# Optimization experiments

Hardware: AMD Instinct MI355X
Metric: run time of the kernel (lower is better)

Reference implementation:

```python
import jax, jax.numpy as jnp
import numpy as np

D_MODEL = 512
N_HEADS = 8
D_K = D_MODEL // N_HEADS
WINDOW = 64
SCALE = 1.0 / np.sqrt(D_K)


def setup_inputs() -> dict:
    key = jax.random.key(0)
    ks = jax.random.split(key, 9)
    B, S = 1, 2048
    s = 1.0 / np.sqrt(D_MODEL)
    inp = {
        "x": jax.random.normal(ks[0], (B, S, D_MODEL), dtype=jnp.float32),
        "Wq": jax.random.normal(ks[1], (D_MODEL, D_MODEL), dtype=jnp.float32) * s,
        "bq": jnp.zeros((D_MODEL,), dtype=jnp.float32),
        "Wk": jax.random.normal(ks[2], (D_MODEL, D_MODEL), dtype=jnp.float32) * s,
        "bk": jnp.zeros((D_MODEL,), dtype=jnp.float32),
        "Wv": jax.random.normal(ks[3], (D_MODEL, D_MODEL), dtype=jnp.float32) * s,
        "bv": jnp.zeros((D_MODEL,), dtype=jnp.float32),
        "Wo": jax.random.normal(ks[4], (D_MODEL, D_MODEL), dtype=jnp.float32) * s,
        "bo": jnp.zeros((D_MODEL,), dtype=jnp.float32),
    }
    return inp


def reference(x, Wq, bq, Wk, bk, Wv, bv, Wo, bo):
    B, S, _ = x.shape
    # projections (torch Linear: x @ W.T + b); split heads -> [B,S,H,dk]
    q = (x @ Wq.T + bq).reshape(B, S, N_HEADS, D_K)
    k = (x @ Wk.T + bk).reshape(B, S, N_HEADS, D_K)
    v = (x @ Wv.T + bv).reshape(B, S, N_HEADS, D_K)

    # banded window indices: position i attends to [i-W, i+W]
    L = 2 * WINDOW + 1
    offsets = jnp.arange(L) - WINDOW                    # [L]
    pos = jnp.arange(S)[:, None] + offsets[None, :]     # [S, L]
    valid = (pos >= 0) & (pos < S)                      # [S, L]
    posc = jnp.clip(pos, 0, S - 1)

    k_w = k[:, posc]                                    # [B, S, L, H, dk]
    v_w = v[:, posc]                                    # [B, S, L, H, dk]

    scores = jnp.einsum("bshd,bslhd->bhsl", q, k_w) * SCALE
    scores = jnp.where(valid[None, None, :, :], scores, -jnp.inf)
    attn = jax.nn.softmax(scores, axis=-1)              # [B, H, S, L]
    out = jnp.einsum("bhsl,bslhd->bshd", attn, v_w)     # [B, S, H, dk]
    out = out.reshape(B, S, D_MODEL)
    return out @ Wo.T + bo
```

## Files before the change

### kernel.cpp

```cpp
#include <hip/hip_runtime.h>
#include <hip/hip_bf16.h>
#include <math.h>

#define S_LEN  2048
#define DMODEL 512
#define NHEADS 8
#define DK     64
#define WIN    64

static constexpr float SCALE = 0.125f;

typedef short bf16x8 __attribute__((ext_vector_type(8)));
typedef float f32x4  __attribute__((ext_vector_type(4)));

__device__ __forceinline__ short bfh(float v)
{
    __hip_bfloat16 b = __float2bfloat16(v);
    return *reinterpret_cast<short*>(&b);
}
__device__ __forceinline__ float bf2f(short s)
{
    __hip_bfloat16 b = *reinterpret_cast<__hip_bfloat16*>(&s);
    return __bfloat162float(b);
}
__device__ __forceinline__ void split1(float v, short& h, short& l)
{
    h = bfh(v);
    l = bfh(v - bf2f(h));
}

__device__ __forceinline__ void dma16(const void* g, void* l)
{
    __builtin_amdgcn_global_load_lds(
        (const __attribute__((address_space(1))) unsigned int*)g,
        (__attribute__((address_space(3))) unsigned int*)l, 16, 0, 0);
}

__global__ __launch_bounds__(256)
void prep(const float* __restrict__ x,
          const float* __restrict__ wq, const float* __restrict__ wk,
          const float* __restrict__ wv, const float* __restrict__ wo,
          short* __restrict__ xh, short* __restrict__ xl,
          short* __restrict__ wqb, short* __restrict__ wkb,
          short* __restrict__ wvb, short* __restrict__ wob)
{
    const int z = blockIdx.z;
    if (z == 0) {
        for (int i = blockIdx.x * 256 + threadIdx.x; i < 262144; i += gridDim.x * 256) {
            const float4 v = ((const float4*)x)[i];
            short4 h4, l4;
            split1(v.x, h4.x, l4.x);
            split1(v.y, h4.y, l4.y);
            split1(v.z, h4.z, l4.z);
            split1(v.w, h4.w, l4.w);
            ((short4*)xh)[i] = h4;
            ((short4*)xl)[i] = l4;
        }
    } else {
        const float* s; short* d;
        switch (z) {
            case 1:  s = wq; d = wqb; break;
            case 2:  s = wk; d = wkb; break;
            case 3:  s = wv; d = wvb; break;
            default: s = wo; d = wob; break;
        }
        for (int i = blockIdx.x * 256 + threadIdx.x; i < 65536; i += gridDim.x * 256) {
            const float4 v = ((const float4*)s)[i];
            short4 o;
            o.x = bfh(v.x); o.y = bfh(v.y); o.z = bfh(v.z); o.w = bfh(v.w);
            ((short4*)d)[i] = o;
        }
    }
}

__global__ __launch_bounds__(128)
void gemm_qkv7(const short* __restrict__ xh, const short* __restrict__ xl,
               const short* __restrict__ wqb, const short* __restrict__ wkb,
               const short* __restrict__ wvb,
               const float* __restrict__ bq, const float* __restrict__ bk,
               const float* __restrict__ bv,
               short* __restrict__ qb, short* __restrict__ kb,
               short* __restrict__ vbt)
{
    __shared__ __align__(16) short sW[64 * 128];

    const int z = blockIdx.z;
    const short* Bg   = (z == 0) ? wqb : (z == 1) ? wkb : wvb;
    const float* bias = (z == 0) ? bq  : (z == 1) ? bk  : bv;
    const int row0 = blockIdx.y * 32;
    const int col0 = blockIdx.x * 64;
    const int tid  = threadIdx.x;
    const int lane = tid & 63;
    const int wv   = tid >> 6;
    const int col  = lane & 15;
    const int quad = lane >> 4;
    const int m    = row0 + wv * 16 + col;

    f32x4 acc[4];
#pragma unroll
    for (int nj = 0; nj < 4; ++nj)
        acc[nj] = (f32x4)0.0f;

    for (int ph = 0; ph < 4; ++ph) {
        __syncthreads();
        for (int i = wv; i < 16; i += 2) {
            const int r = i * 4 + (lane >> 4);
            const int c = lane & 15;
            const int j = c ^ (r & 7);
            dma16(Bg + (size_t)(col0 + r) * 512 + ph * 128 + j * 8, sW + i * 512);
        }
        __syncthreads();

#pragma unroll
        for (int kc = 0; kc < 4; ++kc) {
            const size_t aoff = (size_t)m * 512 + ph * 128 + kc * 32 + quad * 8;
            const bf16x8 ah = *(const bf16x8*)(xh + aoff);
            const bf16x8 al = *(const bf16x8*)(xl + aoff);
#pragma unroll
            for (int nj = 0; nj < 4; ++nj) {
                const int n = nj * 16 + col;
                const int c = kc * 4 + quad;
                const bf16x8 bf = *(const bf16x8*)&sW[n * 128 + (c ^ (n & 7)) * 8];
                acc[nj] = __builtin_amdgcn_mfma_f32_16x16x32_bf16(ah, bf, acc[nj], 0, 0, 0);
                acc[nj] = __builtin_amdgcn_mfma_f32_16x16x32_bf16(al, bf, acc[nj], 0, 0, 0);
            }
        }
    }

#pragma unroll
    for (int nj = 0; nj < 4; ++nj) {
        const int cc = col0 + nj * 16 + col;
        const float bias_v = bias[cc];
#pragma unroll
        for (int e = 0; e < 4; ++e) {
            const int row = row0 + wv * 16 + quad * 4 + e;
            const float val = acc[nj][e] + bias_v;
            if (z == 0) {
                qb[(size_t)row * 512 + cc] = bfh(val);
            } else if (z == 1) {
                kb[(size_t)row * 512 + cc] = bfh(val);
            } else {
                vbt[(size_t)cc * 2048 + row] = bfh(val);
            }
        }
    }
}

__global__ __launch_bounds__(128)
void gemm_out7(const short* __restrict__ ah_g,
               const short* __restrict__ wob, const float* __restrict__ bo,
               float* __restrict__ out)
{
    __shared__ __align__(16) short sW[64 * 128];

    const int row0 = blockIdx.y * 32;
    const int col0 = blockIdx.x * 64;
    const int tid  = threadIdx.x;
    const int lane = tid & 63;
    const int wv   = tid >> 6;
    const int col  = lane & 15;
    const int quad = lane >> 4;
    const int m    = row0 + wv * 16 + col;

    f32x4 acc[4];
#pragma unroll
    for (int nj = 0; nj < 4; ++nj)
        acc[nj] = (f32x4)0.0f;

    for (int ph = 0; ph < 4; ++ph) {
        __syncthreads();
        for (int i = wv; i < 16; i += 2) {
            const int r = i * 4 + (lane >> 4);
            const int c = lane & 15;
            const int j = c ^ (r & 7);
            dma16(wob + (size_t)(col0 + r) * 512 + ph * 128 + j * 8, sW + i * 512);
        }
        __syncthreads();

#pragma unroll
        for (int kc = 0; kc < 4; ++kc) {
            const bf16x8 af = *(const bf16x8*)(ah_g + (size_t)m * 512 + ph * 128 + kc * 32 + quad * 8);
#pragma unroll
            for (int nj = 0; nj < 4; ++nj) {
                const int n = nj * 16 + col;
                const int c = kc * 4 + quad;
                const bf16x8 bf = *(const bf16x8*)&sW[n * 128 + (c ^ (n & 7)) * 8];
                acc[nj] = __builtin_amdgcn_mfma_f32_16x16x32_bf16(af, bf, acc[nj], 0, 0, 0);
            }
        }
    }

#pragma unroll
    for (int nj = 0; nj < 4; ++nj) {
        const int cc = col0 + nj * 16 + col;
        const float bias_v = bo[cc];
#pragma unroll
        for (int e = 0; e < 4; ++e) {
            const int row = row0 + wv * 16 + quad * 4 + e;
            out[(size_t)row * 512 + cc] = acc[nj][e] + bias_v;
        }
    }
}

__global__ __launch_bounds__(256)
void banded_attn6(const short* __restrict__ qb, const short* __restrict__ kb,
                  const short* __restrict__ vbt, short* __restrict__ abh)
{
    __shared__ __align__(16) short VtS[64 * 256];
    __shared__ __align__(16) short KS [192 * 64];
    __shared__ __align__(16) short QS [32 * 64];
    __shared__ float pmax[4][32];
    __shared__ float psum[4][32];
    short* PS = KS;

    const int h    = blockIdx.x;
    const int t0   = blockIdx.y * 32;
    const int tid  = threadIdx.x;
    const int lane = tid & 63;
    const int wv   = tid >> 6;
    const int col  = lane & 15;
    const int quad = lane >> 4;

    {
        const int lr = lane >> 3;
        const int lc = lane & 7;
        for (int i = wv; i < 28; i += 4) {
            const short* src; short* dst; int r;
            if (i < 4) {
                r = i * 8 + lr;
                src = qb + (size_t)(t0 + r) * 512 + h * 64;
                dst = QS + i * 512;
            } else {
                const int g = i - 4;
                r = g * 8 + lr;
                int pos = t0 - 64 + r;
                pos = pos < 0 ? 0 : (pos > 2047 ? 2047 : pos);
                src = kb + (size_t)pos * 512 + h * 64;
                dst = KS + g * 512;
            }
            const int cs = lc ^ (r & 7);
            dma16(src + cs * 8, dst);
        }
        for (int i = wv; i < 32; i += 4) {
            const int q = i * 64 + lane;
            const int d = q >> 5;
            const int b = q & 31;
            const int j0 = (b < 24) ? b : 0;
            const int j = j0 ^ (d & 7);
            int p0 = t0 - 64 + j * 8;
            p0 = p0 < 0 ? 0 : (p0 > 2040 ? 2040 : p0);
            dma16(vbt + (size_t)(h * 64 + d) * 2048 + p0, VtS + i * 512);
        }
    }
    __syncthreads();

    f32x4 sacc[2][3];
#pragma unroll
    for (int mi = 0; mi < 2; ++mi)
#pragma unroll
        for (int nj = 0; nj < 3; ++nj)
            sacc[mi][nj] = (f32x4)0.0f;

#pragma unroll
    for (int ks = 0; ks < 2; ++ks) {
        const int q0 = ks * 4 + quad;
        bf16x8 aq[2];
#pragma unroll
        for (int mi = 0; mi < 2; ++mi) {
            const int mm = mi * 16 + col;
            const int p = q0 ^ (mm & 7);
            aq[mi] = *(const bf16x8*)&QS[mm * 64 + p * 8];
        }
#pragma unroll
        for (int nj = 0; nj < 3; ++nj) {
            const int n = wv * 48 + nj * 16 + col;
            const int p = q0 ^ (n & 7);
            const bf16x8 bkf = *(const bf16x8*)&KS[n * 64 + p * 8];
#pragma unroll
            for (int mi = 0; mi < 2; ++mi)
                sacc[mi][nj] = __builtin_amdgcn_mfma_f32_16x16x32_bf16(aq[mi], bkf, sacc[mi][nj], 0, 0, 0);
        }
    }

    float pv[2][3][4];
#pragma unroll
    for (int mi = 0; mi < 2; ++mi)
#pragma unroll
        for (int nj = 0; nj < 3; ++nj)
#pragma unroll
            for (int e = 0; e < 4; ++e) {
                const int r32 = mi * 16 + quad * 4 + e;
                const int n   = wv * 48 + nj * 16 + col;
                const int pos = t0 - 64 + n;
                const int d   = n - r32;
                const bool valid = (pos >= 0) && (pos < S_LEN) && (d >= 0) && (d <= 128);
                pv[mi][nj][e] = valid ? sacc[mi][nj][e] * SCALE : -__builtin_inff();
            }

#pragma unroll
    for (int mi = 0; mi < 2; ++mi)
#pragma unroll
        for (int e = 0; e < 4; ++e) {
            float mx = fmaxf(fmaxf(pv[mi][0][e], pv[mi][1][e]), pv[mi][2][e]);
#pragma unroll
            for (int off = 1; off < 16; off <<= 1)
                mx = fmaxf(mx, __shfl_xor(mx, off));
            if ((lane & 15) == 0) pmax[wv][mi * 16 + quad * 4 + e] = mx;
        }
    __syncthreads();

#pragma unroll
    for (int mi = 0; mi < 2; ++mi)
#pragma unroll
        for (int e = 0; e < 4; ++e) {
            const int r32 = mi * 16 + quad * 4 + e;
            const float m = fmaxf(fmaxf(pmax[0][r32], pmax[1][r32]),
                                  fmaxf(pmax[2][r32], pmax[3][r32]));
            float ss = 0.f;
#pragma unroll
            for (int nj = 0; nj < 3; ++nj) {
                const float p = __expf(pv[mi][nj][e] - m);
                pv[mi][nj][e] = p;
                ss += p;
            }
#pragma unroll
            for (int off = 1; off < 16; off <<= 1)
                ss += __shfl_xor(ss, off);
            if ((lane & 15) == 0) psum[wv][r32] = ss;
#pragma unroll
            for (int nj = 0; nj < 3; ++nj) {
                const int n = wv * 48 + nj * 16 + col;
                PS[r32 * 200 + n] = bfh(pv[mi][nj][e]);
            }
        }
    __syncthreads();

    const int mi = wv >> 1;
    f32x4 oacc[2];
    oacc[0] = (f32x4)0.0f;
    oacc[1] = (f32x4)0.0f;
#pragma unroll
    for (int ks = 0; ks < 6; ++ks) {
        const bf16x8 pa = *(const bf16x8*)&PS[(mi * 16 + col) * 200 + ks * 32 + quad * 8];
#pragma unroll
        for (int t = 0; t < 2; ++t) {
            const int d = ((wv & 1) * 2 + t) * 16 + col;
            const int j = (ks * 4 + quad) ^ (d & 7);
            const bf16x8 vf = *(const bf16x8*)&VtS[d * 256 + j * 8];
            oacc[t] = __builtin_amdgcn_mfma_f32_16x16x32_bf16(pa, vf, oacc[t], 0, 0, 0);
        }
    }

    float linv[4];
#pragma unroll
    for (int e = 0; e < 4; ++e) {
        const int r32 = mi * 16 + quad * 4 + e;
        linv[e] = 1.0f / (psum[0][r32] + psum[1][r32] + psum[2][r32] + psum[3][r32]);
    }
#pragma unroll
    for (int t = 0; t < 2; ++t) {
        const int nj = (wv & 1) * 2 + t;
#pragma unroll
        for (int e = 0; e < 4; ++e) {
            const int r32 = mi * 16 + quad * 4 + e;
            const float val = oacc[t][e] * linv[e];
            const size_t idx = (size_t)(t0 + r32) * 512 + h * 64 + nj * 16 + col;
            abh[idx] = bfh(val);
        }
    }
}

extern "C" void kernel_launch(void* const* d_in, const int* in_sizes, int n_in,
                              void* d_out, int out_size, void* d_ws, size_t ws_size,
                              hipStream_t stream)
{
    const float* x  = (const float*)d_in[0];
    const float* Wq = (const float*)d_in[1];
    const float* bq = (const float*)d_in[2];
    const float* Wk = (const float*)d_in[3];
    const float* bk = (const float*)d_in[4];
    const float* Wv = (const float*)d_in[5];
    const float* bv = (const float*)d_in[6];
    const float* Wo = (const float*)d_in[7];
    const float* bo = (const float*)d_in[8];
    float* out = (float*)d_out;

    char* ws = (char*)d_ws;
    short* qb  = (short*)(ws);
    short* kb  = (short*)(ws + (2u << 20));
    short* vbt = (short*)(ws + (4u << 20));
    short* abh = (short*)(ws + (6u << 20));
    short* xh  = (short*)(ws + (8u << 20));
    short* xl  = (short*)(ws + (10u << 20));
    short* wqb = (short*)(ws + (12u << 20));
    short* wkb = (short*)(ws + (12u << 20) + 1 * (512u << 10));
    short* wvb = (short*)(ws + (12u << 20) + 2 * (512u << 10));
    short* wob = (short*)(ws + (12u << 20) + 3 * (512u << 10));

    dim3 gp(128, 1, 5);
    prep<<<gp, 256, 0, stream>>>(x, Wq, Wk, Wv, Wo,
                                 xh, xl, wqb, wkb, wvb, wob);

    dim3 gq(DMODEL / 64, S_LEN / 32, 3);
    gemm_qkv7<<<gq, 128, 0, stream>>>(xh, xl, wqb, wkb, wvb,
                                      bq, bk, bv, qb, kb, vbt);

    dim3 ga(NHEADS, S_LEN / 32);
    banded_attn6<<<ga, 256, 0, stream>>>(qb, kb, vbt, abh);

    dim3 go(DMODEL / 64, S_LEN / 32);
    gemm_out7<<<go, 128, 0, stream>>>(abh, wob, bo, out);
}
```

Before: 111.2 us.

## Stage full-K weight tile in LDS once and enlarge GEMM row tiles

Both projection GEMMs now load the entire 64x512 bf16 weight slice into shared memory with a single sync, replacing four K-phases that each had two barriers. Blocks grow to four waves and 64 output rows, so each staged weight tile serves twice as many rows and the grid is halved. The cost is 64KB of LDS per block, which limits occupancy, and fewer blocks in flight to hide latency.

```diff
diff --git a/kernel.cpp b/kernel.cpp
--- a/kernel.cpp
+++ b/kernel.cpp
@@ -73,8 +73,8 @@
     }
 }
 
-__global__ __launch_bounds__(128)
-void gemm_qkv7(const short* __restrict__ xh, const short* __restrict__ xl,
+__global__ __launch_bounds__(256)
+void gemm_qkv8(const short* __restrict__ xh, const short* __restrict__ xl,
                const short* __restrict__ wqb, const short* __restrict__ wkb,
                const short* __restrict__ wvb,
                const float* __restrict__ bq, const float* __restrict__ bk,
@@ -82,12 +82,12 @@
                short* __restrict__ qb, short* __restrict__ kb,
                short* __restrict__ vbt)
 {
-    __shared__ __align__(16) short sW[64 * 128];
+    __shared__ __align__(16) short sW[64 * 512];
 
     const int z = blockIdx.z;
     const short* Bg   = (z == 0) ? wqb : (z == 1) ? wkb : wvb;
     const float* bias = (z == 0) ? bq  : (z == 1) ? bk  : bv;
-    const int row0 = blockIdx.y * 32;
+    const int row0 = blockIdx.y * 64;
     const int col0 = blockIdx.x * 64;
     const int tid  = threadIdx.x;
     const int lane = tid & 63;
@@ -96,34 +96,29 @@
     const int quad = lane >> 4;
     const int m    = row0 + wv * 16 + col;
 
+    for (int i = wv; i < 64; i += 4) {
+        dma16(Bg + (size_t)(col0 + i) * 512 + (size_t)((lane ^ (i & 7)) * 8),
+              sW + i * 512);
+    }
+    __syncthreads();
+
     f32x4 acc[4];
 #pragma unroll
     for (int nj = 0; nj < 4; ++nj)
         acc[nj] = (f32x4)0.0f;
 
-    for (int ph = 0; ph < 4; ++ph) {
-        __syncthreads();
-        for (int i = wv; i < 16; i += 2) {
-            const int r = i * 4 + (lane >> 4);
-            const int c = lane & 15;
-            const int j = c ^ (r & 7);
-            dma16(Bg + (size_t)(col0 + r) * 512 + ph * 128 + j * 8, sW + i * 512);
-        }
-        __syncthreads();
-
-#pragma unroll
-        for (int kc = 0; kc < 4; ++kc) {
-            const size_t aoff = (size_t)m * 512 + ph * 128 + kc * 32 + quad * 8;
-            const bf16x8 ah = *(const bf16x8*)(xh + aoff);
-            const bf16x8 al = *(const bf16x8*)(xl + aoff);
-#pragma unroll
-            for (int nj = 0; nj < 4; ++nj) {
-                const int n = nj * 16 + col;
-                const int c = kc * 4 + quad;
-                const bf16x8 bf = *(const bf16x8*)&sW[n * 128 + (c ^ (n & 7)) * 8];
-                acc[nj] = __builtin_amdgcn_mfma_f32_16x16x32_bf16(ah, bf, acc[nj], 0, 0, 0);
-                acc[nj] = __builtin_amdgcn_mfma_f32_16x16x32_bf16(al, bf, acc[nj], 0, 0, 0);
-            }
+#pragma unroll 4
+    for (int kc = 0; kc < 16; ++kc) {
+        const size_t aoff = (size_t)m * 512 + kc * 32 + quad * 8;
+        const bf16x8 ah = *(const bf16x8*)(xh + aoff);
+        const bf16x8 al = *(const bf16x8*)(xl + aoff);
+#pragma unroll
+        for (int nj = 0; nj < 4; ++nj) {
+            const int n = nj * 16 + col;
+            const int c = kc * 4 + quad;
+            const bf16x8 bf = *(const bf16x8*)&sW[n * 512 + ((c ^ (n & 7)) * 8)];
+            acc[nj] = __builtin_amdgcn_mfma_f32_16x16x32_bf16(ah, bf, acc[nj], 0, 0, 0);
+            acc[nj] = __builtin_amdgcn_mfma_f32_16x16x32_bf16(al, bf, acc[nj], 0, 0, 0);
         }
     }
 
@@ -146,14 +141,14 @@
     }
 }
 
-__global__ __launch_bounds__(128)
-void gemm_out7(const short* __restrict__ ah_g,
+__global__ __launch_bounds__(256)
+void gemm_out8(const short* __restrict__ ah_g,
                const short* __restrict__ wob, const float* __restrict__ bo,
                float* __restrict__ out)
 {
-    __shared__ __align__(16) short sW[64 * 128];
-
-    const int row0 = blockIdx.y * 32;
+    __shared__ __align__(16) short sW[64 * 512];
+
+    const int row0 = blockIdx.y * 64;
     const int col0 = blockIdx.x * 64;
     const int tid  = threadIdx.x;
     const int lane = tid & 63;
@@ -162,31 +157,26 @@
     const int quad = lane >> 4;
     const int m    = row0 + wv * 16 + col;
 
+    for (int i = wv; i < 64; i += 4) {
+        dma16(wob + (size_t)(col0 + i) * 512 + (size_t)((lane ^ (i & 7)) * 8),
+              sW + i * 512);
+    }
+    __syncthreads();
+
     f32x4 acc[4];
 #pragma unroll
     for (int nj = 0; nj < 4; ++nj)
         acc[nj] = (f32x4)0.0f;
 
-    for (int ph = 0; ph < 4; ++ph) {
-        __syncthreads();
-        for (int i = wv; i < 16; i += 2) {
-            const int r = i * 4 + (lane >> 4);
-            const int c = lane & 15;
-            const int j = c ^ (r & 7);
-            dma16(wob + (size_t)(col0 + r) * 512 + ph * 128 + j * 8, sW + i * 512);
-        }
-        __syncthreads();
-
-#pragma unroll
-        for (int kc = 0; kc < 4; ++kc) {
-            const bf16x8 af = *(const bf16x8*)(ah_g + (size_t)m * 512 + ph * 128 + kc * 32 + quad * 8);
-#pragma unroll
-            for (int nj = 0; nj < 4; ++nj) {
-                const int n = nj * 16 + col;
-                const int c = kc * 4 + quad;
-                const bf16x8 bf = *(const bf16x8*)&sW[n * 128 + (c ^ (n & 7)) * 8];
-                acc[nj] = __builtin_amdgcn_mfma_f32_16x16x32_bf16(af, bf, acc[nj], 0, 0, 0);
-            }
+#pragma unroll 4
+    for (int kc = 0; kc < 16; ++kc) {
+        const bf16x8 af = *(const bf16x8*)(ah_g + (size_t)m * 512 + kc * 32 + quad * 8);
+#pragma unroll
+        for (int nj = 0; nj < 4; ++nj) {
+            const int n = nj * 16 + col;
+            const int c = kc * 4 + quad;
+            const bf16x8 bf = *(const bf16x8*)&sW[n * 512 + ((c ^ (n & 7)) * 8)];
+            acc[nj] = __builtin_amdgcn_mfma_f32_16x16x32_bf16(af, bf, acc[nj], 0, 0, 0);
         }
     }
 
@@ -401,13 +391,13 @@
     prep<<<gp, 256, 0, stream>>>(x, Wq, Wk, Wv, Wo,
                                  xh, xl, wqb, wkb, wvb, wob);
 
-    dim3 gq(DMODEL / 64, S_LEN / 32, 3);
-    gemm_qkv7<<<gq, 128, 0, stream>>>(xh, xl, wqb, wkb, wvb,
+    dim3 gq(DMODEL / 64, S_LEN / 64, 3);
+    gemm_qkv8<<<gq, 256, 0, stream>>>(xh, xl, wqb, wkb, wvb,
                                       bq, bk, bv, qb, kb, vbt);
 
     dim3 ga(NHEADS, S_LEN / 32);
     banded_attn6<<<ga, 256, 0, stream>>>(qb, kb, vbt, abh);
 
-    dim3 go(DMODEL / 64, S_LEN / 32);
-    gemm_out7<<<go, 128, 0, stream>>>(abh, wob, bo, out);
-}
+    dim3 go(DMODEL / 64, S_LEN / 64);
+    gemm_out8<<<go, 256, 0, stream>>>(abh, wob, bo, out);
+}
```

Measured after the change: 115.6 us. +4.0%, slower.

## Double-buffer weight tiles in GEMMs and defer V staging in attention

Applied to the files above, without the earlier changes.

Both projection GEMMs now hold two shared-memory weight buffers. The next K-phase is loaded while MFMAs run on the current one, which removes one barrier per phase. The attention kernel issues the V-transpose load after the Q/K barrier, so it can overlap with the QK^T score computation. This doubles GEMM LDS use, which may lower occupancy, and it relies on a later barrier before V is read.

```diff
diff --git a/kernel.cpp b/kernel.cpp
--- a/kernel.cpp
+++ b/kernel.cpp
@@ -74,7 +74,7 @@
 }
 
 __global__ __launch_bounds__(128)
-void gemm_qkv7(const short* __restrict__ xh, const short* __restrict__ xl,
+void gemm_qkv9(const short* __restrict__ xh, const short* __restrict__ xl,
                const short* __restrict__ wqb, const short* __restrict__ wkb,
                const short* __restrict__ wvb,
                const float* __restrict__ bq, const float* __restrict__ bk,
@@ -82,7 +82,7 @@
                short* __restrict__ qb, short* __restrict__ kb,
                short* __restrict__ vbt)
 {
-    __shared__ __align__(16) short sW[64 * 128];
+    __shared__ __align__(16) short sW[2][64 * 128];
 
     const int z = blockIdx.z;
     const short* Bg   = (z == 0) ? wqb : (z == 1) ? wkb : wvb;
@@ -96,21 +96,28 @@
     const int quad = lane >> 4;
     const int m    = row0 + wv * 16 + col;
 
+#define STAGE_W(b, ph)                                                          \
+    for (int i = wv; i < 16; i += 2) {                                          \
+        const int r = i * 4 + (lane >> 4);                                      \
+        const int c = lane & 15;                                                \
+        const int j = c ^ (r & 7);                                              \
+        dma16(Bg + (size_t)(col0 + r) * 512 + (ph) * 128 + j * 8,               \
+              &sW[b][i * 512]);                                                 \
+    }
+
+    STAGE_W(0, 0)
+    __syncthreads();
+
     f32x4 acc[4];
 #pragma unroll
     for (int nj = 0; nj < 4; ++nj)
         acc[nj] = (f32x4)0.0f;
 
     for (int ph = 0; ph < 4; ++ph) {
-        __syncthreads();
-        for (int i = wv; i < 16; i += 2) {
-            const int r = i * 4 + (lane >> 4);
-            const int c = lane & 15;
-            const int j = c ^ (r & 7);
-            dma16(Bg + (size_t)(col0 + r) * 512 + ph * 128 + j * 8, sW + i * 512);
-        }
-        __syncthreads();
-
+        const int b = ph & 1;
+        if (ph < 3) {
+            STAGE_W(b ^ 1, ph + 1)
+        }
 #pragma unroll
         for (int kc = 0; kc < 4; ++kc) {
             const size_t aoff = (size_t)m * 512 + ph * 128 + kc * 32 + quad * 8;
@@ -120,12 +127,14 @@
             for (int nj = 0; nj < 4; ++nj) {
                 const int n = nj * 16 + col;
                 const int c = kc * 4 + quad;
-                const bf16x8 bf = *(const bf16x8*)&sW[n * 128 + (c ^ (n & 7)) * 8];
+                const bf16x8 bf = *(const bf16x8*)&sW[b][n * 128 + (c ^ (n & 7)) * 8];
                 acc[nj] = __builtin_amdgcn_mfma_f32_16x16x32_bf16(ah, bf, acc[nj], 0, 0, 0);
                 acc[nj] = __builtin_amdgcn_mfma_f32_16x16x32_bf16(al, bf, acc[nj], 0, 0, 0);
             }
         }
-    }
+        __syncthreads();
+    }
+#undef STAGE_W
 
 #pragma unroll
     for (int nj = 0; nj < 4; ++nj) {
@@ -147,11 +156,11 @@
 }
 
 __global__ __launch_bounds__(128)
-void gemm_out7(const short* __restrict__ ah_g,
+void gemm_out9(const short* __restrict__ ah_g,
                const short* __restrict__ wob, const float* __restrict__ bo,
                float* __restrict__ out)
 {
-    __shared__ __align__(16) short sW[64 * 128];
+    __shared__ __align__(16) short sW[2][64 * 128];
 
     const int row0 = blockIdx.y * 32;
     const int col0 = blockIdx.x * 64;
@@ -162,21 +171,28 @@
     const int quad = lane >> 4;
     const int m    = row0 + wv * 16 + col;
 
+#define STAGE_W(b, ph)                                                          \
+    for (int i = wv; i < 16; i += 2) {                                          \
+        const int r = i * 4 + (lane >> 4);                                      \
+        const int c = lane & 15;                                                \
+        const int j = c ^ (r & 7);                                              \
+        dma16(wob + (size_t)(col0 + r) * 512 + (ph) * 128 + j * 8,              \
+              &sW[b][i * 512]);                                                 \
+    }
+
+    STAGE_W(0, 0)
+    __syncthreads();
+
     f32x4 acc[4];
 #pragma unroll
     for (int nj = 0; nj < 4; ++nj)
         acc[nj] = (f32x4)0.0f;
 
     for (int ph = 0; ph < 4; ++ph) {
-        __syncthreads();
-        for (int i = wv; i < 16; i += 2) {
-            const int r = i * 4 + (lane >> 4);
-            const int c = lane & 15;
-            const int j = c ^ (r & 7);
-            dma16(wob + (size_t)(col0 + r) * 512 + ph * 128 + j * 8, sW + i * 512);
-        }
-        __syncthreads();
-
+        const int b = ph & 1;
+        if (ph < 3) {
+            STAGE_W(b ^ 1, ph + 1)
+        }
 #pragma unroll
         for (int kc = 0; kc < 4; ++kc) {
             const bf16x8 af = *(const bf16x8*)(ah_g + (size_t)m * 512 + ph * 128 + kc * 32 + quad * 8);
@@ -184,11 +200,13 @@
             for (int nj = 0; nj < 4; ++nj) {
                 const int n = nj * 16 + col;
                 const int c = kc * 4 + quad;
-                const bf16x8 bf = *(const bf16x8*)&sW[n * 128 + (c ^ (n & 7)) * 8];
+                const bf16x8 bf = *(const bf16x8*)&sW[b][n * 128 + (c ^ (n & 7)) * 8];
                 acc[nj] = __builtin_amdgcn_mfma_f32_16x16x32_bf16(af, bf, acc[nj], 0, 0, 0);
             }
         }
-    }
+        __syncthreads();
+    }
+#undef STAGE_W
 
 #pragma unroll
     for (int nj = 0; nj < 4; ++nj) {
@@ -203,7 +221,7 @@
 }
 
 __global__ __launch_bounds__(256)
-void banded_attn6(const short* __restrict__ qb, const short* __restrict__ kb,
+void banded_attn7(const short* __restrict__ qb, const short* __restrict__ kb,
                   const short* __restrict__ vbt, short* __restrict__ abh)
 {
     __shared__ __align__(16) short VtS[64 * 256];
@@ -241,18 +259,19 @@
             const int cs = lc ^ (r & 7);
             dma16(src + cs * 8, dst);
         }
-        for (int i = wv; i < 32; i += 4) {
-            const int q = i * 64 + lane;
-            const int d = q >> 5;
-            const int b = q & 31;
-            const int j0 = (b < 24) ? b : 0;
-            const int j = j0 ^ (d & 7);
-            int p0 = t0 - 64 + j * 8;
-            p0 = p0 < 0 ? 0 : (p0 > 2040 ? 2040 : p0);
-            dma16(vbt + (size_t)(h * 64 + d) * 2048 + p0, VtS + i * 512);
-        }
     }
     __syncthreads();
+
+    for (int i = wv; i < 32; i += 4) {
+        const int q = i * 64 + lane;
+        const int d = q >> 5;
+        const int b = q & 31;
+        const int j0 = (b < 24) ? b : 0;
+        const int j = j0 ^ (d & 7);
+        int p0 = t0 - 64 + j * 8;
+        p0 = p0 < 0 ? 0 : (p0 > 2040 ? 2040 : p0);
+        dma16(vbt + (size_t)(h * 64 + d) * 2048 + p0, VtS + i * 512);
+    }
 
     f32x4 sacc[2][3];
 #pragma unroll
@@ -402,12 +421,12 @@
                                  xh, xl, wqb, wkb, wvb, wob);
 
     dim3 gq(DMODEL / 64, S_LEN / 32, 3);
-    gemm_qkv7<<<gq, 128, 0, stream>>>(xh, xl, wqb, wkb, wvb,
+    gemm_qkv9<<<gq, 128, 0, stream>>>(xh, xl, wqb, wkb, wvb,
                                       bq, bk, bv, qb, kb, vbt);
 
     dim3 ga(NHEADS, S_LEN / 32);
-    banded_attn6<<<ga, 256, 0, stream>>>(qb, kb, vbt, abh);
+    banded_attn7<<<ga, 256, 0, stream>>>(qb, kb, vbt, abh);
 
     dim3 go(DMODEL / 64, S_LEN / 32);
-    gemm_out7<<<go, 128, 0, stream>>>(abh, wob, bo, out);
-}
+    gemm_out9<<<go, 128, 0, stream>>>(abh, wob, bo, out);
+}
```

After: 115.2 us. 3.6% more time.
